# Kernel optimization log

Measured on AMD Instinct MI355X. Metric: run time of the kernel, lower is better.

## Reference

```python
import jax, jax.numpy as jnp
import numpy as np

H = W = 2048        # voxel grid
P0 = 0.1            # occupancy density
EPS = 1e-5          # BatchNorm eps (torch default)


def _grid(rs, cs):
    g = np.full((H, W), -1, np.int64)
    g[rs, cs] = np.arange(rs.size)
    return g


def _conv_map(g, rs, cs, s):
    # kernel map for 3x3 conv at tensor stride s: offsets {-s,0,s}^2, -1 = missing neighbor
    maps = []
    for dr in (-s, 0, s):
        for dc in (-s, 0, s):
            r2, c2 = rs + dr, cs + dc
            ok = (r2 >= 0) & (r2 < H) & (c2 >= 0) & (c2 < W)
            m = np.full(rs.size, -1, np.int64)
            m[ok] = g[r2[ok], c2[ok]]
            maps.append(m)
    return np.stack(maps, 1)  # [N, 9]


def _pool_map(g, rs, cs, s):
    # 2x2 max pool stride 2 at tensor stride s: out coords = floor to multiples of 2s
    out = np.unique(np.stack([rs - rs % (2 * s), cs - cs % (2 * s)], 1), axis=0)
    maps = []
    for dr in (0, s):
        for dc in (0, s):
            r2, c2 = out[:, 0] + dr, out[:, 1] + dc
            ok = (r2 < H) & (c2 < W)
            m = np.full(out.shape[0], -1, np.int64)
            m[ok] = g[r2[ok], c2[ok]]
            maps.append(m)
    return out, np.stack(maps, 1)  # coords, [N_out, 4]


def _build_maps():
    rng = np.random.default_rng(0)
    n0 = int(H * W * P0)
    flat = rng.choice(H * W, size=n0, replace=False)
    flat.sort()
    rs0, cs0 = np.divmod(flat, W)
    g0 = _grid(rs0, cs0)
    nbr0 = _conv_map(g0, rs0, cs0, 1)
    c1, pmap1 = _pool_map(g0, rs0, cs0, 1)
    g1 = _grid(c1[:, 0], c1[:, 1])
    nbr1 = _conv_map(g1, c1[:, 0], c1[:, 1], 2)
    c2, pmap2 = _pool_map(g1, c1[:, 0], c1[:, 1], 2)
    return n0, nbr0, pmap1, nbr1, pmap2, c2.shape[0]


def setup_inputs() -> dict:
    n0, nbr0, pmap1, nbr1, pmap2, n2 = _build_maps()
    key = jax.random.key(0)
    k0, k1, k2, k3 = jax.random.split(key, 4)
    f0 = jax.random.normal(k0, (n0, 1), jnp.float32)
    W1 = jax.random.normal(k1, (9, 1, 8), jnp.float32) * 0.3
    W2 = jax.random.normal(k2, (9, 8, 16), jnp.float32) * 0.12
    Wfc = jax.random.normal(k3, (16, 2), jnp.float32) * 0.25
    return dict(
        f0=f0, W1=W1, b1=jnp.zeros((8,), jnp.float32),
        gamma1=jnp.ones((8,), jnp.float32), beta1=jnp.zeros((8,), jnp.float32),
        W2=W2, b2=jnp.zeros((16,), jnp.float32),
        gamma2=jnp.ones((16,), jnp.float32), beta2=jnp.zeros((16,), jnp.float32),
        Wfc=Wfc, bfc=jnp.zeros((2,), jnp.float32),
        nbr0=jnp.asarray(nbr0), pmap1=jnp.asarray(pmap1),
        nbr1=jnp.asarray(nbr1), pmap2=jnp.asarray(pmap2),
    )


def _sparse_conv(f, nbr, Wk, b):
    # gather-matmul-scatter: missing neighbors contribute zero
    n = f.shape[0]
    fpad = jnp.concatenate([f, jnp.zeros((1, f.shape[1]), f.dtype)], 0)
    g = fpad[jnp.where(nbr < 0, n, nbr)]  # [N_out, 9, C_in]
    return jnp.einsum('nkc,kcd->nd', g, Wk) + b


def _bn_relu(x, gamma, beta):
    mu = x.mean(0)
    var = x.var(0)  # biased, as torch BN normalization
    return jax.nn.relu((x - mu) * jax.lax.rsqrt(var + EPS) * gamma + beta)


def _max_pool(f, pmap):
    # max over existing children only (every output has >= 1 child)
    n = f.shape[0]
    fpad = jnp.concatenate([f, jnp.full((1, f.shape[1]), -jnp.inf, f.dtype)], 0)
    return fpad[jnp.where(pmap < 0, n, pmap)].max(1)


def reference(f0, W1, b1, gamma1, beta1, W2, b2, gamma2, beta2, Wfc, bfc,
              nbr0, pmap1, nbr1, pmap2):
    x = _bn_relu(_sparse_conv(f0, nbr0, W1, b1), gamma1, beta1)
    x = _max_pool(x, pmap1)
    x = _bn_relu(_sparse_conv(x, nbr1, W2, b2), gamma2, beta2)
    x = _max_pool(x, pmap2)
    return x @ Wfc + bfc
```

## Files before the change

### kernel.cpp

```cpp
#include <hip/hip_runtime.h>

#define EPS 1e-5f
#define NSLOT 64

__device__ __forceinline__ float waveReduceSum(float v) {
    #pragma unroll
    for (int off = 32; off > 0; off >>= 1)
        v += __shfl_down(v, off, 64);
    return v;
}

template <int NV>
__device__ __forceinline__ float statReduce(float (&v)[NV], int lane) {
    #pragma unroll
    for (int b = 0; (1 << b) < NV; ++b) {
        const int d = 1 << b;
        const bool hi = (lane >> b) & 1;
        #pragma unroll
        for (int i = 0; i < (NV >> (b + 1)); ++i) {
            float kept = hi ? v[2 * i + 1] : v[2 * i];
            float sent = hi ? v[2 * i] : v[2 * i + 1];
            float recv = __shfl_xor(sent, d, 64);
            v[i] = kept + recv;
        }
    }
    float r = v[0];
    #pragma unroll
    for (int d = NV; d < 64; d <<= 1)
        r += __shfl_xor(r, d, 64);
    return r;
}

__global__ __launch_bounds__(256) void k_zero(float4* __restrict__ slots) {
    const float4 z4 = {0.f, 0.f, 0.f, 0.f};
    #pragma unroll
    for (int q = 0; q < 4; ++q)
        slots[q * 256 + threadIdx.x] = z4;
}

__global__ __launch_bounds__(256) void k_conv1(
        const float* __restrict__ f0, const float* __restrict__ W1,
        const float* __restrict__ b1, const int* __restrict__ nbr0,
        float* __restrict__ x1, float* __restrict__ slots, int n0) {
    __shared__ float sred[16];
    int t = threadIdx.x;
    int lane = t & 63;
    if (t < 16) sred[t] = 0.f;
    __syncthreads();

    int n = blockIdx.x * blockDim.x + t;
    bool valid = (n < n0);
    int nn = valid ? n : (n0 - 1);

    int idx[9];
    #pragma unroll
    for (int k = 0; k < 9; ++k) idx[k] = nbr0[(size_t)nn * 9 + k];
    float v[9];
    #pragma unroll
    for (int k = 0; k < 9; ++k) {
        float f = f0[idx[k] >= 0 ? idx[k] : 0];
        v[k] = (idx[k] >= 0) ? f : 0.f;
    }

    float acc[8];
    #pragma unroll
    for (int c = 0; c < 8; ++c) acc[c] = b1[c];
    #pragma unroll
    for (int k = 0; k < 9; ++k)
        #pragma unroll
        for (int c = 0; c < 8; ++c) acc[c] = fmaf(v[k], W1[k * 8 + c], acc[c]);

    if (valid) {
        float4 lo = {acc[0], acc[1], acc[2], acc[3]};
        float4 hi = {acc[4], acc[5], acc[6], acc[7]};
        float4* dst = (float4*)(x1 + (size_t)n * 8);
        dst[0] = lo; dst[1] = hi;
    } else {
        #pragma unroll
        for (int c = 0; c < 8; ++c) acc[c] = 0.f;
    }

    float red[16];
    #pragma unroll
    for (int c = 0; c < 8; ++c) {
        red[c] = acc[c];
        red[8 + c] = acc[c] * acc[c];
    }
    float tot = statReduce<16>(red, lane);
    if (lane < 16) atomicAdd(&sred[lane], tot);
    __syncthreads();
    if (t < 16) {
        float* slot = slots + (size_t)(blockIdx.x & (NSLOT - 1)) * 64;
        atomicAdd(&slot[t], sred[t]);
    }
}

__global__ __launch_bounds__(256) void k_pool1(
        const float* __restrict__ x1, const int* __restrict__ pmap1,
        const float* __restrict__ slots, const float* __restrict__ gamma1,
        const float* __restrict__ beta1, float* __restrict__ p1,
        int n1, float invn) {
    __shared__ float sstat[16];
    int t = threadIdx.x;
    if (t < 64) {
        const float4* s4 = (const float4*)(slots + (size_t)t * 64);
        float4 a = s4[0], b = s4[1], c4 = s4[2], d = s4[3];
        float vals[16] = {a.x, a.y, a.z, a.w, b.x, b.y, b.z, b.w,
                          c4.x, c4.y, c4.z, c4.w, d.x, d.y, d.z, d.w};
        #pragma unroll
        for (int c = 0; c < 16; ++c) {
            float s = waveReduceSum(vals[c]);
            if (t == 0) sstat[c] = s;
        }
    }
    __syncthreads();

    int i = blockIdx.x * blockDim.x + t;
    if (i >= n1) return;

    float m[8], sc[8], bb[8];
    #pragma unroll
    for (int c = 0; c < 8; ++c) {
        float mu  = sstat[c] * invn;
        float var = sstat[8 + c] * invn - mu * mu;
        m[c]  = mu;
        sc[c] = rsqrtf(var + EPS) * gamma1[c];
        bb[c] = beta1[c];
    }

    int4 pm = ((const int4*)pmap1)[i];
    int idx[4] = {pm.x, pm.y, pm.z, pm.w};
    float best[8];
    #pragma unroll
    for (int c = 0; c < 8; ++c) best[c] = 0.f;
    #pragma unroll
    for (int k = 0; k < 4; ++k) {
        int j = idx[k] >= 0 ? idx[k] : 0;
        const float4* src = (const float4*)(x1 + (size_t)j * 8);
        float4 lo = src[0], hi = src[1];
        float v[8] = {lo.x, lo.y, lo.z, lo.w, hi.x, hi.y, hi.z, hi.w};
        #pragma unroll
        for (int c = 0; c < 8; ++c) {
            float z = fmaxf(fmaf(v[c] - m[c], sc[c], bb[c]), 0.f);
            z = (idx[k] >= 0) ? z : 0.f;
            best[c] = fmaxf(best[c], z);
        }
    }
    float4 lo = {best[0], best[1], best[2], best[3]};
    float4 hi = {best[4], best[5], best[6], best[7]};
    float4* dst = (float4*)(p1 + (size_t)i * 8);
    dst[0] = lo; dst[1] = hi;
}

__global__ __launch_bounds__(256, 4) void k_conv2(
        const float* __restrict__ p1, const float* __restrict__ W2,
        const float* __restrict__ b2, const int* __restrict__ nbr1,
        float* __restrict__ x2, float* __restrict__ slots, int n1) {
    __shared__ float sred[32];
    int t = threadIdx.x;
    int lane = t & 63;
    if (t < 32) sred[t] = 0.f;
    __syncthreads();

    int n = blockIdx.x * blockDim.x + t;
    bool valid = (n < n1);
    int nn = valid ? n : (n1 - 1);

    int idx[9];
    #pragma unroll
    for (int k = 0; k < 9; ++k) idx[k] = nbr1[(size_t)nn * 9 + k];

    float acc[16];
    #pragma unroll
    for (int c = 0; c < 16; ++c) acc[c] = b2[c];

    #pragma unroll
    for (int k = 0; k < 9; ++k) {
        const float4* src = (const float4*)(p1 + (size_t)(idx[k] >= 0 ? idx[k] : 0) * 8);
        float4 lo = src[0], hi = src[1];
        if (idx[k] < 0) {
            lo = make_float4(0.f, 0.f, 0.f, 0.f);
            hi = make_float4(0.f, 0.f, 0.f, 0.f);
        }
        float g[8] = {lo.x, lo.y, lo.z, lo.w, hi.x, hi.y, hi.z, hi.w};
        #pragma unroll
        for (int ci = 0; ci < 8; ++ci) {
            #pragma unroll
            for (int c = 0; c < 16; ++c)
                acc[c] = fmaf(g[ci], W2[(k * 8 + ci) * 16 + c], acc[c]);
        }
    }

    if (valid) {
        float4* dst = (float4*)(x2 + (size_t)n * 16);
        #pragma unroll
        for (int q4 = 0; q4 < 4; ++q4) {
            float4 v = {acc[q4 * 4], acc[q4 * 4 + 1], acc[q4 * 4 + 2], acc[q4 * 4 + 3]};
            dst[q4] = v;
        }
    } else {
        #pragma unroll
        for (int c = 0; c < 16; ++c) acc[c] = 0.f;
    }

    float red[32];
    #pragma unroll
    for (int c = 0; c < 16; ++c) {
        red[c] = acc[c];
        red[16 + c] = acc[c] * acc[c];
    }
    float tot = statReduce<32>(red, lane);
    if (lane < 32) atomicAdd(&sred[lane], tot);
    __syncthreads();
    if (t < 32) {
        float* slot = slots + (size_t)(blockIdx.x & (NSLOT - 1)) * 64;
        atomicAdd(&slot[16 + t], sred[t]);
    }
}

__global__ __launch_bounds__(256) void k_pool2_fc(
        const float* __restrict__ x2, const int* __restrict__ pmap2,
        const float* __restrict__ slots, const float* __restrict__ gamma2,
        const float* __restrict__ beta2, const float* __restrict__ Wfc,
        const float* __restrict__ bfc, float* __restrict__ out,
        int n2, float invn) {
    __shared__ float sstat[32];
    int t = threadIdx.x;
    if (t < 64) {
        const float4* s4 = (const float4*)(slots + (size_t)t * 64 + 16);
        float vals[32];
        #pragma unroll
        for (int q = 0; q < 8; ++q) {
            float4 a = s4[q];
            vals[q * 4 + 0] = a.x; vals[q * 4 + 1] = a.y;
            vals[q * 4 + 2] = a.z; vals[q * 4 + 3] = a.w;
        }
        #pragma unroll
        for (int c = 0; c < 32; ++c) {
            float s = waveReduceSum(vals[c]);
            if (t == 0) sstat[c] = s;
        }
    }
    __syncthreads();

    int i = blockIdx.x * blockDim.x + t;
    if (i >= n2) return;

    float m[16], sc[16], bb[16];
    #pragma unroll
    for (int c = 0; c < 16; ++c) {
        float mu  = sstat[c] * invn;
        float var = sstat[16 + c] * invn - mu * mu;
        m[c]  = mu;
        sc[c] = rsqrtf(var + EPS) * gamma2[c];
        bb[c] = beta2[c];
    }

    int4 pm = ((const int4*)pmap2)[i];
    int idx[4] = {pm.x, pm.y, pm.z, pm.w};
    float best[16];
    #pragma unroll
    for (int c = 0; c < 16; ++c) best[c] = 0.f;
    #pragma unroll
    for (int k = 0; k < 4; ++k) {
        int j = idx[k] >= 0 ? idx[k] : 0;
        const float4* src = (const float4*)(x2 + (size_t)j * 16);
        #pragma unroll
        for (int q4 = 0; q4 < 4; ++q4) {
            float4 v4 = src[q4];
            float v[4] = {v4.x, v4.y, v4.z, v4.w};
            #pragma unroll
            for (int c = 0; c < 4; ++c) {
                int cc = q4 * 4 + c;
                float z = fmaxf(fmaf(v[c] - m[cc], sc[cc], bb[cc]), 0.f);
                z = (idx[k] >= 0) ? z : 0.f;
                best[cc] = fmaxf(best[cc], z);
            }
        }
    }
    float o0 = bfc[0], o1 = bfc[1];
    #pragma unroll
    for (int c = 0; c < 16; ++c) {
        o0 = fmaf(best[c], Wfc[c * 2 + 0], o0);
        o1 = fmaf(best[c], Wfc[c * 2 + 1], o1);
    }
    out[(size_t)i * 2 + 0] = o0;
    out[(size_t)i * 2 + 1] = o1;
}

extern "C" void kernel_launch(void* const* d_in, const int* in_sizes, int n_in,
                              void* d_out, int out_size, void* d_ws, size_t ws_size,
                              hipStream_t stream) {
    const float* f0     = (const float*)d_in[0];
    const float* W1     = (const float*)d_in[1];
    const float* b1     = (const float*)d_in[2];
    const float* gamma1 = (const float*)d_in[3];
    const float* beta1  = (const float*)d_in[4];
    const float* W2     = (const float*)d_in[5];
    const float* b2     = (const float*)d_in[6];
    const float* gamma2 = (const float*)d_in[7];
    const float* beta2  = (const float*)d_in[8];
    const float* Wfc    = (const float*)d_in[9];
    const float* bfc    = (const float*)d_in[10];
    const int*   nbr0   = (const int*)d_in[11];
    const int*   pmap1  = (const int*)d_in[12];
    const int*   nbr1   = (const int*)d_in[13];
    const int*   pmap2  = (const int*)d_in[14];

    const int n0 = in_sizes[0];
    const int n1 = in_sizes[12] / 4;
    const int n2 = in_sizes[14] / 4;

    float* ws    = (float*)d_ws;
    float* slots = ws;
    float* x1    = ws + (size_t)NSLOT * 64;
    float* p1    = x1 + (size_t)n0 * 8;
    float* x2    = p1 + (size_t)n1 * 8;

    const int B = 256;
    k_zero<<<1, B, 0, stream>>>((float4*)slots);
    k_conv1<<<(n0 + B - 1) / B, B, 0, stream>>>(f0, W1, b1, nbr0, x1, slots, n0);
    k_pool1<<<(n1 + B - 1) / B, B, 0, stream>>>(x1, pmap1, slots, gamma1, beta1, p1,
                                                n1, 1.0f / (float)n0);
    k_conv2<<<(n1 + B - 1) / B, B, 0, stream>>>(p1, W2, b2, nbr1, x2, slots, n1);
    k_pool2_fc<<<(n2 + B - 1) / B, B, 0, stream>>>(x2, pmap2, slots, gamma2, beta2,
                                                   Wfc, bfc, (float*)d_out,
                                                   n2, 1.0f / (float)n1);
}
```

Measured before the change: 72.96 us.

## Store intermediate activations x1 and p1 in fp16, precompute BN1 scale/shift

```diff
diff --git a/kernel.cpp b/kernel.cpp
--- a/kernel.cpp
+++ b/kernel.cpp
@@ -1,4 +1,5 @@
 #include <hip/hip_runtime.h>
+#include <hip/hip_fp16.h>
 
 #define EPS 1e-5f
 #define NSLOT 64
@@ -31,17 +32,36 @@
     return r;
 }
 
-__global__ __launch_bounds__(256) void k_zero(float4* __restrict__ slots) {
+__device__ __forceinline__ void unpack8(float4 raw, float* g) {
+    const __half2* hp = reinterpret_cast<const __half2*>(&raw);
+    #pragma unroll
+    for (int q = 0; q < 4; ++q) {
+        float2 f = __half22float2(hp[q]);
+        g[2 * q] = f.x; g[2 * q + 1] = f.y;
+    }
+}
+
+__device__ __forceinline__ float4 pack8(const float* g) {
+    __half2 hp[4];
+    #pragma unroll
+    for (int q = 0; q < 4; ++q)
+        hp[q] = __floats2half2_rn(g[2 * q], g[2 * q + 1]);
+    return *reinterpret_cast<float4*>(hp);
+}
+
+__global__ __launch_bounds__(256) void k_zero(float4* __restrict__ slots,
+                                              float4* __restrict__ p1zrow) {
     const float4 z4 = {0.f, 0.f, 0.f, 0.f};
     #pragma unroll
     for (int q = 0; q < 4; ++q)
         slots[q * 256 + threadIdx.x] = z4;
-}
-
-__global__ __launch_bounds__(256) void k_conv1(
+    if (threadIdx.x == 0) p1zrow[0] = z4;
+}
+
+__global__ __launch_bounds__(256, 4) void k_conv1(
         const float* __restrict__ f0, const float* __restrict__ W1,
         const float* __restrict__ b1, const int* __restrict__ nbr0,
-        float* __restrict__ x1, float* __restrict__ slots, int n0) {
+        float4* __restrict__ x1h, float* __restrict__ slots, int n0) {
     __shared__ float sred[16];
     int t = threadIdx.x;
     int lane = t & 63;
@@ -70,12 +90,8 @@
         #pragma unroll
         for (int c = 0; c < 8; ++c) acc[c] = fmaf(v[k], W1[k * 8 + c], acc[c]);
 
-    if (valid) {
-        float4 lo = {acc[0], acc[1], acc[2], acc[3]};
-        float4 hi = {acc[4], acc[5], acc[6], acc[7]};
-        float4* dst = (float4*)(x1 + (size_t)n * 8);
-        dst[0] = lo; dst[1] = hi;
-    } else {
+    if (valid) x1h[n] = pack8(acc);
+    else {
         #pragma unroll
         for (int c = 0; c < 8; ++c) acc[c] = 0.f;
     }
@@ -89,44 +105,36 @@
     float tot = statReduce<16>(red, lane);
     if (lane < 16) atomicAdd(&sred[lane], tot);
     __syncthreads();
+    if (t < 16)
+        atomicAdd(&slots[(size_t)(blockIdx.x & (NSLOT - 1)) * 64 + t], sred[t]);
+}
+
+__global__ __launch_bounds__(64) void k_bn1stats(
+        const float* __restrict__ slots, const float* __restrict__ gamma1,
+        const float* __restrict__ beta1, float* __restrict__ stats, float invn0) {
+    __shared__ float st[16];
+    int t = threadIdx.x;
     if (t < 16) {
-        float* slot = slots + (size_t)(blockIdx.x & (NSLOT - 1)) * 64;
-        atomicAdd(&slot[t], sred[t]);
-    }
-}
-
-__global__ __launch_bounds__(256) void k_pool1(
-        const float* __restrict__ x1, const int* __restrict__ pmap1,
-        const float* __restrict__ slots, const float* __restrict__ gamma1,
-        const float* __restrict__ beta1, float* __restrict__ p1,
-        int n1, float invn) {
-    __shared__ float sstat[16];
-    int t = threadIdx.x;
-    if (t < 64) {
-        const float4* s4 = (const float4*)(slots + (size_t)t * 64);
-        float4 a = s4[0], b = s4[1], c4 = s4[2], d = s4[3];
-        float vals[16] = {a.x, a.y, a.z, a.w, b.x, b.y, b.z, b.w,
-                          c4.x, c4.y, c4.z, c4.w, d.x, d.y, d.z, d.w};
-        #pragma unroll
-        for (int c = 0; c < 16; ++c) {
-            float s = waveReduceSum(vals[c]);
-            if (t == 0) sstat[c] = s;
-        }
-    }
-    __syncthreads();
-
-    int i = blockIdx.x * blockDim.x + t;
+        float s = 0.f;
+        #pragma unroll 8
+        for (int k = 0; k < NSLOT; ++k) s += slots[(size_t)k * 64 + t];
+        st[t] = s;
+    }
+    __syncthreads();
+    if (t < 8) {
+        float mu  = st[t] * invn0;
+        float var = st[8 + t] * invn0 - mu * mu;
+        float sc  = rsqrtf(var + EPS) * gamma1[t];
+        stats[t]     = sc;
+        stats[8 + t] = beta1[t] - sc * mu;
+    }
+}
+
+__global__ __launch_bounds__(256, 4) void k_pool1(
+        const float4* __restrict__ x1h, const int* __restrict__ pmap1,
+        const float* __restrict__ stats, float4* __restrict__ p1h, int n1) {
+    int i = blockIdx.x * blockDim.x + threadIdx.x;
     if (i >= n1) return;
-
-    float m[8], sc[8], bb[8];
-    #pragma unroll
-    for (int c = 0; c < 8; ++c) {
-        float mu  = sstat[c] * invn;
-        float var = sstat[8 + c] * invn - mu * mu;
-        m[c]  = mu;
-        sc[c] = rsqrtf(var + EPS) * gamma1[c];
-        bb[c] = beta1[c];
-    }
 
     int4 pm = ((const int4*)pmap1)[i];
     int idx[4] = {pm.x, pm.y, pm.z, pm.w};
@@ -135,25 +143,21 @@
     for (int c = 0; c < 8; ++c) best[c] = 0.f;
     #pragma unroll
     for (int k = 0; k < 4; ++k) {
-        int j = idx[k] >= 0 ? idx[k] : 0;
-        const float4* src = (const float4*)(x1 + (size_t)j * 8);
-        float4 lo = src[0], hi = src[1];
-        float v[8] = {lo.x, lo.y, lo.z, lo.w, hi.x, hi.y, hi.z, hi.w};
+        float4 raw = x1h[idx[k] >= 0 ? idx[k] : 0];
+        float v[8];
+        unpack8(raw, v);
         #pragma unroll
         for (int c = 0; c < 8; ++c) {
-            float z = fmaxf(fmaf(v[c] - m[c], sc[c], bb[c]), 0.f);
+            float z = fmaxf(fmaf(v[c], stats[c], stats[8 + c]), 0.f);
             z = (idx[k] >= 0) ? z : 0.f;
             best[c] = fmaxf(best[c], z);
         }
     }
-    float4 lo = {best[0], best[1], best[2], best[3]};
-    float4 hi = {best[4], best[5], best[6], best[7]};
-    float4* dst = (float4*)(p1 + (size_t)i * 8);
-    dst[0] = lo; dst[1] = hi;
+    p1h[i] = pack8(best);
 }
 
 __global__ __launch_bounds__(256, 4) void k_conv2(
-        const float* __restrict__ p1, const float* __restrict__ W2,
+        const float4* __restrict__ p1h, const float* __restrict__ W2,
         const float* __restrict__ b2, const int* __restrict__ nbr1,
         float* __restrict__ x2, float* __restrict__ slots, int n1) {
     __shared__ float sred[32];
@@ -168,7 +172,10 @@
 
     int idx[9];
     #pragma unroll
-    for (int k = 0; k < 9; ++k) idx[k] = nbr1[(size_t)nn * 9 + k];
+    for (int k = 0; k < 9; ++k) {
+        int j = nbr1[(size_t)nn * 9 + k];
+        idx[k] = (j >= 0) ? j : n1;
+    }
 
     float acc[16];
     #pragma unroll
@@ -176,13 +183,9 @@
 
     #pragma unroll
     for (int k = 0; k < 9; ++k) {
-        const float4* src = (const float4*)(p1 + (size_t)(idx[k] >= 0 ? idx[k] : 0) * 8);
-        float4 lo = src[0], hi = src[1];
-        if (idx[k] < 0) {
-            lo = make_float4(0.f, 0.f, 0.f, 0.f);
-            hi = make_float4(0.f, 0.f, 0.f, 0.f);
-        }
-        float g[8] = {lo.x, lo.y, lo.z, lo.w, hi.x, hi.y, hi.z, hi.w};
+        float4 raw = p1h[idx[k]];
+        float g[8];
+        unpack8(raw, g);
         #pragma unroll
         for (int ci = 0; ci < 8; ++ci) {
             #pragma unroll
@@ -194,10 +197,9 @@
     if (valid) {
         float4* dst = (float4*)(x2 + (size_t)n * 16);
         #pragma unroll
-        for (int q4 = 0; q4 < 4; ++q4) {
-            float4 v = {acc[q4 * 4], acc[q4 * 4 + 1], acc[q4 * 4 + 2], acc[q4 * 4 + 3]};
-            dst[q4] = v;
-        }
+        for (int q4 = 0; q4 < 4; ++q4)
+            dst[q4] = make_float4(acc[q4 * 4], acc[q4 * 4 + 1],
+                                  acc[q4 * 4 + 2], acc[q4 * 4 + 3]);
     } else {
         #pragma unroll
         for (int c = 0; c < 16; ++c) acc[c] = 0.f;
@@ -212,10 +214,8 @@
     float tot = statReduce<32>(red, lane);
     if (lane < 32) atomicAdd(&sred[lane], tot);
     __syncthreads();
-    if (t < 32) {
-        float* slot = slots + (size_t)(blockIdx.x & (NSLOT - 1)) * 64;
-        atomicAdd(&slot[16 + t], sred[t]);
-    }
+    if (t < 32)
+        atomicAdd(&slots[(size_t)(blockIdx.x & (NSLOT - 1)) * 64 + 16 + t], sred[t]);
 }
 
 __global__ __launch_bounds__(256) void k_pool2_fc(
@@ -311,18 +311,19 @@
     const int n1 = in_sizes[12] / 4;
     const int n2 = in_sizes[14] / 4;
 
-    float* ws    = (float*)d_ws;
-    float* slots = ws;
-    float* x1    = ws + (size_t)NSLOT * 64;
-    float* p1    = x1 + (size_t)n0 * 8;
-    float* x2    = p1 + (size_t)n1 * 8;
+    float*  ws    = (float*)d_ws;
+    float*  slots = ws;
+    float*  stats = ws + (size_t)NSLOT * 64;
+    float4* x1h   = (float4*)(stats + 16);
+    float4* p1h   = x1h + n0;
+    float*  x2    = (float*)(p1h + n1 + 1);
 
     const int B = 256;
-    k_zero<<<1, B, 0, stream>>>((float4*)slots);
-    k_conv1<<<(n0 + B - 1) / B, B, 0, stream>>>(f0, W1, b1, nbr0, x1, slots, n0);
-    k_pool1<<<(n1 + B - 1) / B, B, 0, stream>>>(x1, pmap1, slots, gamma1, beta1, p1,
-                                                n1, 1.0f / (float)n0);
-    k_conv2<<<(n1 + B - 1) / B, B, 0, stream>>>(p1, W2, b2, nbr1, x2, slots, n1);
+    k_zero<<<1, B, 0, stream>>>((float4*)slots, p1h + n1);
+    k_conv1<<<(n0 + B - 1) / B, B, 0, stream>>>(f0, W1, b1, nbr0, x1h, slots, n0);
+    k_bn1stats<<<1, 64, 0, stream>>>(slots, gamma1, beta1, stats, 1.0f / (float)n0);
+    k_pool1<<<(n1 + B - 1) / B, B, 0, stream>>>(x1h, pmap1, stats, p1h, n1);
+    k_conv2<<<(n1 + B - 1) / B, B, 0, stream>>>(p1h, W2, b2, nbr1, x2, slots, n1);
     k_pool2_fc<<<(n2 + B - 1) / B, B, 0, stream>>>(x2, pmap2, slots, gamma2, beta2,
                                                    Wfc, bfc, (float*)d_out,
                                                    n2, 1.0f / (float)n1);
```

New measurement: 75.80 us. 1.04x slower.
